# Performance work log

Measured on AMD Instinct MI355X. Metric: run time of the kernel, lower is better.

Reference implementation:

```python
import jax, jax.numpy as jnp
import numpy as np

N_NODES = 50000


def _gcn_conv(x, edge_index, W, b, num_nodes):
    """PyG GCNConv: h = D^{-1/2} (A + I) D^{-1/2} (x W) + b."""
    # add self loops
    loops = jnp.arange(num_nodes, dtype=edge_index.dtype)
    src = jnp.concatenate([edge_index[0], loops])  # [E + N]
    dst = jnp.concatenate([edge_index[1], loops])
    # symmetric degree normalization (edge weight 1.0, incl. self loops)
    deg = jax.ops.segment_sum(jnp.ones_like(src, dtype=x.dtype), dst,
                              num_segments=num_nodes)
    dinv = jnp.where(deg > 0, jax.lax.rsqrt(deg), 0.0)
    norm = dinv[src] * dinv[dst]  # [E + N]
    h = x @ W  # [N, H] dense GEMM first (PyG applies lin before propagate)
    msgs = h[src] * norm[:, None]  # gather + scale, [E + N, H]
    out = jax.ops.segment_sum(msgs, dst, num_segments=num_nodes)  # scatter-add
    return out + b


def setup_inputs() -> dict:
    key = jax.random.key(0)
    ks = jax.random.split(key, 6)
    F_in, H = 100, 1024
    state = jax.random.normal(ks[0], (N_NODES, F_in, 1), dtype=jnp.float32)
    edge_index = jax.random.randint(ks[1], (2, 200000), 0, N_NODES, dtype=jnp.int64)
    W1 = jax.random.normal(ks[2], (F_in, H), dtype=jnp.float32) / np.sqrt(F_in)
    b1 = jax.random.normal(ks[3], (H,), dtype=jnp.float32) * 0.01
    W_head = jax.random.normal(ks[4], (H, 1), dtype=jnp.float32) / np.sqrt(H)
    b_head = jax.random.normal(ks[5], (1,), dtype=jnp.float32) * 0.01
    return {"state": state, "edge_index": edge_index, "W1": W1, "b1": b1,
            "W_head": W_head, "b_head": b_head}


def reference(state, edge_index, W1, b1, W_head, b_head):
    x = state.reshape(state.shape[0], state.shape[1])  # (N, F, 1) -> (N, F)
    h = _gcn_conv(x, edge_index, W1, b1, N_NODES)      # GCNConv 100 -> 1024
    return h @ W_head + b_head                          # linear head -> (N, 1)
```

## Files before the change

kernel.cpp:

```cpp
#include <hip/hip_runtime.h>


#define N_NODES 50000
#define F_IN    100
#define H_DIM   1024
#define N_EDGES 200000

__global__ void __launch_bounds__(256)
k0_fold_zero(const float* __restrict__ W1, const float* __restrict__ b1,
             const float* __restrict__ Wh, const float* __restrict__ bh,
             float* __restrict__ w, float* __restrict__ c,
             float4* __restrict__ deg_zero)
{
    const int b = blockIdx.x;
    const int t = threadIdx.x;
    if (b <= 100) {
        const float* row = (b < 100) ? (W1 + (size_t)b * H_DIM) : b1;
        float s = 0.0f;
        #pragma unroll
        for (int k = 0; k < H_DIM / 256; ++k) {
            const int h = t + 256 * k;
            s += row[h] * Wh[h];
        }
        #pragma unroll
        for (int off = 32; off > 0; off >>= 1) s += __shfl_down(s, off, 64);
        __shared__ float red[4];
        const int wave = t >> 6, lane = t & 63;
        if (lane == 0) red[wave] = s;
        __syncthreads();
        if (t == 0) {
            const float tot = red[0] + red[1] + red[2] + red[3];
            if (b < 100) w[b] = tot;
            else         *c  = tot + bh[0];
        }
    } else {
        const int g = (b - 101) * 256 + t;
        if (g < N_NODES / 4)
            deg_zero[g] = make_float4(0.f, 0.f, 0.f, 0.f);
    }
}

__global__ void __launch_bounds__(256)
k1_deg_seed_score(const float* __restrict__ x, const int* __restrict__ ei,
                  const float* __restrict__ w, const float* __restrict__ c,
                  unsigned* __restrict__ deg, float* __restrict__ sbuf,
                  float4* __restrict__ out4)
{
    const int tid   = blockIdx.x * 256 + threadIdx.x;
    const int gwave = tid >> 6;
    const int lane  = tid & 63;

    if (tid < N_EDGES / 4) {
        const int4 d4 = ((const int4*)(ei + N_EDGES))[tid];
        atomicAdd(&deg[d4.x], 1u);
        atomicAdd(&deg[d4.y], 1u);
        atomicAdd(&deg[d4.z], 1u);
        atomicAdd(&deg[d4.w], 1u);
    } else if (tid < N_EDGES / 4 + N_NODES / 4) {
        const float cv = c[0];
        out4[tid - N_EDGES / 4] = make_float4(cv, cv, cv, cv);
    }

    if (gwave < N_NODES) {
        const float* row = x + (size_t)gwave * F_IN;
        float s = row[lane] * w[lane];
        if (lane < F_IN - 64) s += row[64 + lane] * w[64 + lane];
        #pragma unroll
        for (int off = 32; off > 0; off >>= 1) s += __shfl_down(s, off, 64);
        if (lane == 0) sbuf[gwave] = s;
    }
}

__global__ void __launch_bounds__(256)
k2_scatter(const int* __restrict__ ei, const unsigned* __restrict__ deg,
           const float* __restrict__ sbuf, float* __restrict__ out)
{
    const int tid = blockIdx.x * 256 + threadIdx.x;
    if (tid < N_EDGES / 2) {
        const int2 s2 = ((const int2*)ei)[tid];
        const int2 d2 = ((const int2*)(ei + N_EDGES))[tid];
        const float u0 = sbuf[s2.x] * rsqrtf((float)deg[s2.x] + 1.0f)
                                    * rsqrtf((float)deg[d2.x] + 1.0f);
        const float u1 = sbuf[s2.y] * rsqrtf((float)deg[s2.y] + 1.0f)
                                    * rsqrtf((float)deg[d2.y] + 1.0f);
        unsafeAtomicAdd(&out[d2.x], u0);
        unsafeAtomicAdd(&out[d2.y], u1);
    } else if (tid < N_EDGES / 2 + N_NODES) {
        const int i = tid - N_EDGES / 2;
        const float dv = rsqrtf((float)deg[i] + 1.0f);
        unsafeAtomicAdd(&out[i], dv * dv * sbuf[i]);
    }
}

extern "C" void kernel_launch(void* const* d_in, const int* in_sizes, int n_in,
                              void* d_out, int out_size, void* d_ws, size_t ws_size,
                              hipStream_t stream)
{
    const float* x   = (const float*)d_in[0];
    const int*   ei  = (const int*)  d_in[1];
    const float* W1  = (const float*)d_in[2];
    const float* b1  = (const float*)d_in[3];
    const float* Wh  = (const float*)d_in[4];
    const float* bh  = (const float*)d_in[5];
    float*       out = (float*)d_out;

    float*    ws_f = (float*)d_ws;
    float*    w    = ws_f;
    float*    c    = ws_f + 100;
    unsigned* deg  = (unsigned*)(ws_f + 128);
    float*    sbuf = ws_f + 128 + N_NODES;

    k0_fold_zero<<<101 + (N_NODES / 4 + 255) / 256, 256, 0, stream>>>(
        W1, b1, Wh, bh, w, c, (float4*)deg);
    k1_deg_seed_score<<<(N_NODES * 64 + 255) / 256, 256, 0, stream>>>(
        x, ei, w, c, deg, sbuf, (float4*)out);
    k2_scatter<<<(N_EDGES / 2 + N_NODES + 255) / 256, 256, 0, stream>>>(
        ei, deg, sbuf, out);
}
```

Baseline: 103.1 us.

## Move degree counting earlier and precompute per-node normalization before edge scatter

Degree counting moves into the first kernel, and zeroing becomes a hipMemsetAsync. The score kernel can then compute dinv, the pre-scaled score and the self-loop term per node, and write the output directly instead of seeding it and adding atomically. The scatter kernel now does one gather and one atomic per edge, with no per-edge rsqrt and no self-loop atomics. In exchange it adds a memset launch and an extra dinv buffer.

```diff
diff --git a/kernel.cpp b/kernel.cpp
--- a/kernel.cpp
+++ b/kernel.cpp
@@ -7,10 +7,11 @@
 #define N_EDGES 200000
 
 __global__ void __launch_bounds__(256)
-k0_fold_zero(const float* __restrict__ W1, const float* __restrict__ b1,
-             const float* __restrict__ Wh, const float* __restrict__ bh,
-             float* __restrict__ w, float* __restrict__ c,
-             float4* __restrict__ deg_zero)
+k0_fold_count(const float* __restrict__ W1, const float* __restrict__ b1,
+              const float* __restrict__ Wh, const float* __restrict__ bh,
+              const int* __restrict__ ei,
+              float* __restrict__ w, float* __restrict__ c,
+              unsigned* __restrict__ deg)
 {
     const int b = blockIdx.x;
     const int t = threadIdx.x;
@@ -34,61 +35,53 @@
             else         *c  = tot + bh[0];
         }
     } else {
-        const int g = (b - 101) * 256 + t;
-        if (g < N_NODES / 4)
-            deg_zero[g] = make_float4(0.f, 0.f, 0.f, 0.f);
+        const int tid = (b - 101) * 256 + t;
+        if (tid < N_EDGES / 4) {
+            const int4 d4 = ((const int4*)(ei + N_EDGES))[tid];
+            atomicAdd(&deg[d4.x], 1u);
+            atomicAdd(&deg[d4.y], 1u);
+            atomicAdd(&deg[d4.z], 1u);
+            atomicAdd(&deg[d4.w], 1u);
+        }
     }
 }
 
 __global__ void __launch_bounds__(256)
-k1_deg_seed_score(const float* __restrict__ x, const int* __restrict__ ei,
-                  const float* __restrict__ w, const float* __restrict__ c,
-                  unsigned* __restrict__ deg, float* __restrict__ sbuf,
-                  float4* __restrict__ out4)
+k1_score_finalize(const float* __restrict__ x, const float* __restrict__ w,
+                  const float* __restrict__ c, const unsigned* __restrict__ deg,
+                  float* __restrict__ tbuf, float* __restrict__ dinv,
+                  float* __restrict__ out)
 {
     const int tid   = blockIdx.x * 256 + threadIdx.x;
     const int gwave = tid >> 6;
     const int lane  = tid & 63;
 
-    if (tid < N_EDGES / 4) {
-        const int4 d4 = ((const int4*)(ei + N_EDGES))[tid];
-        atomicAdd(&deg[d4.x], 1u);
-        atomicAdd(&deg[d4.y], 1u);
-        atomicAdd(&deg[d4.z], 1u);
-        atomicAdd(&deg[d4.w], 1u);
-    } else if (tid < N_EDGES / 4 + N_NODES / 4) {
-        const float cv = c[0];
-        out4[tid - N_EDGES / 4] = make_float4(cv, cv, cv, cv);
-    }
+    float dgv = 0.0f;
+    if (lane == 0) dgv = (float)deg[gwave];
 
-    if (gwave < N_NODES) {
-        const float* row = x + (size_t)gwave * F_IN;
-        float s = row[lane] * w[lane];
-        if (lane < F_IN - 64) s += row[64 + lane] * w[64 + lane];
-        #pragma unroll
-        for (int off = 32; off > 0; off >>= 1) s += __shfl_down(s, off, 64);
-        if (lane == 0) sbuf[gwave] = s;
+    const float* row = x + (size_t)gwave * F_IN;
+    float s = row[lane] * w[lane];
+    if (lane < F_IN - 64) s += row[64 + lane] * w[64 + lane];
+    #pragma unroll
+    for (int off = 32; off > 0; off >>= 1) s += __shfl_down(s, off, 64);
+
+    if (lane == 0) {
+        const float dv = rsqrtf(dgv + 1.0f);
+        tbuf[gwave] = dv * s;
+        dinv[gwave] = dv;
+        out[gwave]  = c[0] + dv * dv * s;
     }
 }
 
 __global__ void __launch_bounds__(256)
-k2_scatter(const int* __restrict__ ei, const unsigned* __restrict__ deg,
-           const float* __restrict__ sbuf, float* __restrict__ out)
+k2_scatter(const int* __restrict__ ei, const float* __restrict__ tbuf,
+           const float* __restrict__ dinv, float* __restrict__ out)
 {
     const int tid = blockIdx.x * 256 + threadIdx.x;
-    if (tid < N_EDGES / 2) {
-        const int2 s2 = ((const int2*)ei)[tid];
-        const int2 d2 = ((const int2*)(ei + N_EDGES))[tid];
-        const float u0 = sbuf[s2.x] * rsqrtf((float)deg[s2.x] + 1.0f)
-                                    * rsqrtf((float)deg[d2.x] + 1.0f);
-        const float u1 = sbuf[s2.y] * rsqrtf((float)deg[s2.y] + 1.0f)
-                                    * rsqrtf((float)deg[d2.y] + 1.0f);
-        unsafeAtomicAdd(&out[d2.x], u0);
-        unsafeAtomicAdd(&out[d2.y], u1);
-    } else if (tid < N_EDGES / 2 + N_NODES) {
-        const int i = tid - N_EDGES / 2;
-        const float dv = rsqrtf((float)deg[i] + 1.0f);
-        unsafeAtomicAdd(&out[i], dv * dv * sbuf[i]);
+    if (tid < N_EDGES) {
+        const int s = ei[tid];
+        const int d = ei[N_EDGES + tid];
+        unsafeAtomicAdd(&out[d], tbuf[s] * dinv[d]);
     }
 }
 
@@ -108,12 +101,13 @@
     float*    w    = ws_f;
     float*    c    = ws_f + 100;
     unsigned* deg  = (unsigned*)(ws_f + 128);
-    float*    sbuf = ws_f + 128 + N_NODES;
+    float*    tbuf = ws_f + 128 + N_NODES;
+    float*    dinv = ws_f + 128 + 2 * N_NODES;
 
-    k0_fold_zero<<<101 + (N_NODES / 4 + 255) / 256, 256, 0, stream>>>(
-        W1, b1, Wh, bh, w, c, (float4*)deg);
-    k1_deg_seed_score<<<(N_NODES * 64 + 255) / 256, 256, 0, stream>>>(
-        x, ei, w, c, deg, sbuf, (float4*)out);
-    k2_scatter<<<(N_EDGES / 2 + N_NODES + 255) / 256, 256, 0, stream>>>(
-        ei, deg, sbuf, out);
+    hipMemsetAsync(deg, 0, N_NODES * sizeof(unsigned), stream);
+    k0_fold_count<<<101 + (N_EDGES / 4 + 255) / 256, 256, 0, stream>>>(
+        W1, b1, Wh, bh, ei, w, c, deg);
+    k1_score_finalize<<<(N_NODES * 64) / 256, 256, 0, stream>>>(
+        x, w, c, deg, tbuf, dinv, out);
+    k2_scatter<<<(N_EDGES + 255) / 256, 256, 0, stream>>>(ei, tbuf, dinv, out);
 }
```

After: 107.3 us. 1.04x slower.

## Fuse three stages into one cooperative kernel with grid-wide syncs

Applied to the files above, without the earlier changes.

Replaces the three back-to-back launches (weight fold plus degree zeroing, degree count plus node scoring, edge scatter) with a single cooperative kernel. Grid-wide barriers separate the phases. The node-scoring phase becomes a grid-stride loop over a persistent grid sized from occupancy, clamped between 640 and 1024 blocks. This removes inter-kernel launch gaps and drains, at the cost of two grid.sync barriers and fewer threads for the scoring pass. The original three-kernel path stays as a fallback if the cooperative launch fails.

```diff
diff --git a/kernel.cpp b/kernel.cpp
--- a/kernel.cpp
+++ b/kernel.cpp
@@ -1,10 +1,97 @@
 #include <hip/hip_runtime.h>
+#include <hip/hip_cooperative_groups.h>
+
+namespace cg = cooperative_groups;
 
 
 #define N_NODES 50000
 #define F_IN    100
 #define H_DIM   1024
 #define N_EDGES 200000
+
+__global__ void __launch_bounds__(256)
+k_fused(const float* __restrict__ x, const int* __restrict__ ei,
+        const float* __restrict__ W1, const float* __restrict__ b1,
+        const float* __restrict__ Wh, const float* __restrict__ bh,
+        float* __restrict__ w, float* __restrict__ c,
+        unsigned* __restrict__ deg, float* __restrict__ sbuf,
+        float* __restrict__ out)
+{
+    const cg::grid_group grid = cg::this_grid();
+    const int b   = blockIdx.x;
+    const int t   = threadIdx.x;
+    const int tid = b * 256 + t;
+
+    if (b <= 100) {
+        const float* row = (b < 100) ? (W1 + (size_t)b * H_DIM) : b1;
+        float s = 0.0f;
+        #pragma unroll
+        for (int k = 0; k < H_DIM / 256; ++k) {
+            const int h = t + 256 * k;
+            s += row[h] * Wh[h];
+        }
+        #pragma unroll
+        for (int off = 32; off > 0; off >>= 1) s += __shfl_down(s, off, 64);
+        __shared__ float red[4];
+        const int wave = t >> 6, lane = t & 63;
+        if (lane == 0) red[wave] = s;
+        __syncthreads();
+        if (t == 0) {
+            const float tot = red[0] + red[1] + red[2] + red[3];
+            if (b < 100) w[b] = tot;
+            else         *c  = tot + bh[0];
+        }
+    } else if (b <= 149) {
+        const int g = (b - 101) * 256 + t;
+        if (g < N_NODES / 4)
+            ((float4*)deg)[g] = make_float4(0.f, 0.f, 0.f, 0.f);
+    }
+
+    grid.sync();
+
+    if (tid < N_EDGES / 4) {
+        const int4 d4 = ((const int4*)(ei + N_EDGES))[tid];
+        atomicAdd(&deg[d4.x], 1u);
+        atomicAdd(&deg[d4.y], 1u);
+        atomicAdd(&deg[d4.z], 1u);
+        atomicAdd(&deg[d4.w], 1u);
+    } else if (tid < N_EDGES / 4 + N_NODES / 4) {
+        const float cv = c[0];
+        ((float4*)out)[tid - N_EDGES / 4] = make_float4(cv, cv, cv, cv);
+    }
+    {
+        const int nwaves = (gridDim.x << 8) >> 6;
+        const int gw0    = tid >> 6;
+        const int lane   = tid & 63;
+        const float wl  = w[lane];
+        const float wh2 = (lane < F_IN - 64) ? w[64 + lane] : 0.0f;
+        for (int n = gw0; n < N_NODES; n += nwaves) {
+            const float* row = x + (size_t)n * F_IN;
+            float s = row[lane] * wl;
+            if (lane < F_IN - 64) s += row[64 + lane] * wh2;
+            #pragma unroll
+            for (int off = 32; off > 0; off >>= 1) s += __shfl_down(s, off, 64);
+            if (lane == 0) sbuf[n] = s;
+        }
+    }
+
+    grid.sync();
+
+    if (tid < N_EDGES / 2) {
+        const int2 s2 = ((const int2*)ei)[tid];
+        const int2 d2 = ((const int2*)(ei + N_EDGES))[tid];
+        const float u0 = sbuf[s2.x] * rsqrtf((float)deg[s2.x] + 1.0f)
+                                    * rsqrtf((float)deg[d2.x] + 1.0f);
+        const float u1 = sbuf[s2.y] * rsqrtf((float)deg[s2.y] + 1.0f)
+                                    * rsqrtf((float)deg[d2.y] + 1.0f);
+        unsafeAtomicAdd(&out[d2.x], u0);
+        unsafeAtomicAdd(&out[d2.y], u1);
+    } else if (tid < N_EDGES / 2 + N_NODES) {
+        const int i = tid - N_EDGES / 2;
+        const float dv = rsqrtf((float)deg[i] + 1.0f);
+        unsafeAtomicAdd(&out[i], dv * dv * sbuf[i]);
+    }
+}
 
 __global__ void __launch_bounds__(256)
 k0_fold_zero(const float* __restrict__ W1, const float* __restrict__ b1,
@@ -110,10 +197,29 @@
     unsigned* deg  = (unsigned*)(ws_f + 128);
     float*    sbuf = ws_f + 128 + N_NODES;
 
-    k0_fold_zero<<<101 + (N_NODES / 4 + 255) / 256, 256, 0, stream>>>(
-        W1, b1, Wh, bh, w, c, (float4*)deg);
-    k1_deg_seed_score<<<(N_NODES * 64 + 255) / 256, 256, 0, stream>>>(
-        x, ei, w, c, deg, sbuf, (float4*)out);
-    k2_scatter<<<(N_EDGES / 2 + N_NODES + 255) / 256, 256, 0, stream>>>(
-        ei, deg, sbuf, out);
-}
+    static int gblocks = 0;
+    if (gblocks == 0) {
+        int occ = 0;
+        if (hipOccupancyMaxActiveBlocksPerMultiprocessor(&occ, k_fused, 256, 0)
+                == hipSuccess && occ > 0)
+            gblocks = occ * 256;
+        else
+            gblocks = 1024;
+        if (gblocks > 1024) gblocks = 1024;
+        if (gblocks < 640)  gblocks = 640;
+    }
+
+    void* args[] = {(void*)&x, (void*)&ei, (void*)&W1, (void*)&b1,
+                    (void*)&Wh, (void*)&bh, (void*)&w, (void*)&c,
+                    (void*)&deg, (void*)&sbuf, (void*)&out};
+    hipError_t e = hipLaunchCooperativeKernel(k_fused, dim3(gblocks), dim3(256),
+                                              args, 0, stream);
+    if (e != hipSuccess) {
+        k0_fold_zero<<<101 + (N_NODES / 4 + 255) / 256, 256, 0, stream>>>(
+            W1, b1, Wh, bh, w, c, (float4*)deg);
+        k1_deg_seed_score<<<(N_NODES * 64 + 255) / 256, 256, 0, stream>>>(
+            x, ei, w, c, deg, sbuf, (float4*)out);
+        k2_scatter<<<(N_EDGES / 2 + N_NODES + 255) / 256, 256, 0, stream>>>(
+            ei, deg, sbuf, out);
+    }
+}
```

Result: slower. 351.6 us (+241.0%).
